# Optimization experiments

Measured on AMD Instinct MI355X. Metric: run time of the kernel, lower is better.

## Reference

```python
import jax, jax.numpy as jnp
import numpy as np

B, L, D, H = 2, 8192, 1024, 16
HD = D // H  # head_dim = 64


def setup_inputs() -> dict:
    key = jax.random.key(0)
    ks = jax.random.split(key, 5)
    s = 1.0 / np.sqrt(D)
    return {
        "x": jax.random.normal(ks[0], (B, L, D), dtype=jnp.float32),
        "Wq": jax.random.normal(ks[1], (D, D), dtype=jnp.float32) * s,
        "bq": jnp.zeros((D,), dtype=jnp.float32),
        "Wk": jax.random.normal(ks[2], (D, D), dtype=jnp.float32) * s,
        "bk": jnp.zeros((D,), dtype=jnp.float32),
        "Wv": jax.random.normal(ks[3], (D, D), dtype=jnp.float32) * s,
        "bv": jnp.zeros((D,), dtype=jnp.float32),
        "Wo": jax.random.normal(ks[4], (D, D), dtype=jnp.float32) * s,
        "bo": jnp.zeros((D,), dtype=jnp.float32),
    }


def _rotary(seq_len, dim):
    pos = jnp.arange(seq_len, dtype=jnp.float32)
    freq = 1.0 / (10000.0 ** (jnp.arange(0, dim, 2, dtype=jnp.float32) / dim))
    ang = pos[:, None] * freq[None, :]               # (L, dim/2)
    sin, cos = jnp.sin(ang), jnp.cos(ang)
    # interleave-duplicate: stack((s,s),-1).reshape(L,dim)  (matches torch code)
    sin = jnp.stack((sin, sin), axis=-1).reshape(seq_len, dim)
    cos = jnp.stack((cos, cos), axis=-1).reshape(seq_len, dim)
    return sin, cos


def _rotate_half(t):
    t1, t2 = jnp.split(t, 2, axis=-1)
    return jnp.concatenate([-t2, t1], axis=-1)


def reference(x, Wq, bq, Wk, bk, Wv, bv, Wo, bo):
    b, l, d = x.shape
    q = (x @ Wq + bq).reshape(b, l, H, HD)
    k = (x @ Wk + bk).reshape(b, l, H, HD)
    v = (x @ Wv + bv).reshape(b, l, H, HD)

    sin, cos = _rotary(l, HD)
    sin = sin[None, :, None, :]  # (1, L, 1, HD)
    cos = cos[None, :, None, :]
    q = q * cos + _rotate_half(q) * sin
    k = k * cos + _rotate_half(k) * sin

    # NOTE: faithful to original — heads NOT transposed to (B,H,L,HD),
    # so scores are (B, L, H, H): attention mixes across heads per position.
    scores = jnp.einsum('blhd,bled->blhe', q, k) / jnp.sqrt(jnp.float32(HD))
    w = jax.nn.softmax(scores, axis=-1)              # dropout = identity (eval)
    out = jnp.einsum('blhe,bled->blhd', w, v).reshape(b, l, d)
    return out @ Wo + bo
```

## Files before the change

kernel.cpp:

```cpp
#include <hip/hip_runtime.h>
#include <hip/hip_bf16.h>

typedef __bf16 bf16_t;
typedef __bf16 bf16x8 __attribute__((ext_vector_type(8)));
typedef float f32x4 __attribute__((ext_vector_type(4)));

#define SEQ_L 8192
#define DMODEL 1024
#define NHEAD 16
#define HDIM 64
static constexpr int MROWS = 2 * SEQ_L;

__device__ __forceinline__ void async_cp16(const bf16_t* g, bf16_t* l) {
  __builtin_amdgcn_global_load_lds(
      (__attribute__((address_space(1))) void*)(void*)(g),
      (__attribute__((address_space(3))) void*)(void*)(l), 16, 0, 0);
}
__device__ __forceinline__ void wg_barrier() { __builtin_amdgcn_s_barrier(); }

__global__ __launch_bounds__(256) void f32_to_bf16_k(const float* __restrict__ in,
                                                     bf16_t* __restrict__ out, int n) {
  int i = (blockIdx.x * 256 + threadIdx.x) * 8;
  if (i >= n) return;
  float4 a = *(const float4*)(in + i);
  float4 b = *(const float4*)(in + i + 4);
  bf16x8 o;
  o[0] = (__bf16)a.x; o[1] = (__bf16)a.y; o[2] = (__bf16)a.z; o[3] = (__bf16)a.w;
  o[4] = (__bf16)b.x; o[5] = (__bf16)b.y; o[6] = (__bf16)b.z; o[7] = (__bf16)b.w;
  *(bf16x8*)(out + i) = o;
}

__global__ __launch_bounds__(256) void w_to_bt_k(
    const float* __restrict__ W0, const float* __restrict__ W1,
    const float* __restrict__ W2, const float* __restrict__ W3,
    bf16_t* __restrict__ T0, bf16_t* __restrict__ T1,
    bf16_t* __restrict__ T2, bf16_t* __restrict__ T3) {
  __shared__ float tile[32][33];
  const int z = blockIdx.z;
  const float* W = (z == 0) ? W0 : (z == 1) ? W1 : (z == 2) ? W2 : W3;
  bf16_t* T = (z == 0) ? T0 : (z == 1) ? T1 : (z == 2) ? T2 : T3;
  const int bx = blockIdx.x, by = blockIdx.y;
  const int tx = threadIdx.x, ty = threadIdx.y;
#pragma unroll
  for (int r = 0; r < 4; ++r)
    tile[ty + r * 8][tx] = W[(size_t)(by * 32 + ty + r * 8) * DMODEL + bx * 32 + tx];
  __syncthreads();
#pragma unroll
  for (int r = 0; r < 4; ++r)
    T[(size_t)(bx * 32 + ty + r * 8) * DMODEL + by * 32 + tx] = (bf16_t)tile[tx][ty + r * 8];
}

__global__ __launch_bounds__(256) void rope_tab_k(float2* __restrict__ tab) {
  int i = blockIdx.x * 256 + threadIdx.x;
  int pos = i >> 5, j = i & 31;
  double freq = pow(10000.0, -(double)j / 32.0);
  double ang = (double)pos * freq;
  tab[i] = make_float2((float)cos(ang), (float)sin(ang));
}

template <int MODE>
__global__ __launch_bounds__(512, 2) void gemm256(
    const bf16_t* __restrict__ A, const bf16_t* __restrict__ Bt,
    const float* __restrict__ b0, const float* __restrict__ b1,
    const float* __restrict__ b2, const float2* __restrict__ rope,
    void* __restrict__ O0, void* __restrict__ O1, void* __restrict__ O2) {
  constexpr int K = DMODEL;
  constexpr int KT = K / 64;
  __shared__ bf16_t As_[2][256 * 64];
  __shared__ bf16_t Bs_[2][256 * 64];
  const int tid = threadIdx.x;
  const int lane = tid & 63;
  const int wave = tid >> 6;
  const int wm = wave >> 2;
  const int wn = wave & 3;
  const size_t row0 = (size_t)blockIdx.x * 256;
  const int col0 = blockIdx.y * 256;
  const int fr = lane & 15;
  const int fkb = (lane >> 4) * 16;

  const int srow = tid >> 3;
  const int schunk = (tid & 7) ^ ((tid >> 3) & 7);
  const bf16_t* gA = A + (row0 + srow) * K + schunk * 8;
  const bf16_t* gB = Bt + ((size_t)col0 + srow) * K + schunk * 8;

#define STAGE_A(j, h)                                  \
  do {                                                 \
    const bf16_t* _g = gA + ((h)*128) * K + (j)*64;    \
    bf16_t* _l = &As_[(j)&1][(h)*8192 + tid * 8];      \
    async_cp16(_g, _l);                                \
    async_cp16(_g + 64 * K, _l + 4096);                \
  } while (0)
#define STAGE_B(j, h)                                  \
  do {                                                 \
    const bf16_t* _g = gB + ((h)*128) * K + (j)*64;    \
    bf16_t* _l = &Bs_[(j)&1][(h)*8192 + tid * 8];      \
    async_cp16(_g, _l);                                \
    async_cp16(_g + 64 * K, _l + 4096);                \
  } while (0)
#define RD(base, row, kh)                                                    \
  (*(const bf16x8*)((const char*)(base) +                                    \
                    (((row)*128 + ((kh)*64 + fkb)) ^ (((row)&7) << 4))))
#define VMCNT(n) asm volatile("s_waitcnt vmcnt(" #n ")")

  f32x4 acc[8][4] = {};
  bf16x8 af[4][2], bf0[2][2], bf1[2][2];

  STAGE_A(0, 0); STAGE_A(0, 1);
  STAGE_B(0, 0); STAGE_B(0, 1);
  STAGE_B(1, 0); STAGE_B(1, 1);
  STAGE_A(1, 0);
  VMCNT(6);
  wg_barrier();

  for (int m = 0; m < KT; ++m) {
    const bf16_t* Ac = &As_[m & 1][0];
    const bf16_t* Bc = &Bs_[m & 1][0];
#pragma unroll
    for (int f = 0; f < 4; ++f) {
      const int r = wm * 128 + f * 16 + fr;
      af[f][0] = RD(Ac, r, 0);
      af[f][1] = RD(Ac, r, 1);
    }
#pragma unroll
    for (int f = 0; f < 2; ++f) {
      const int r = wn * 64 + f * 16 + fr;
      bf0[f][0] = RD(Bc, r, 0);
      bf0[f][1] = RD(Bc, r, 1);
    }
    if (m + 1 < KT) STAGE_A(m + 1, 1);
    wg_barrier();
    __builtin_amdgcn_s_setprio(1);
#pragma unroll
    for (int f = 0; f < 4; ++f)
#pragma unroll
      for (int n = 0; n < 2; ++n)
#pragma unroll
        for (int kh = 0; kh < 2; ++kh)
          acc[f][n] = __builtin_amdgcn_mfma_f32_16x16x32_bf16(af[f][kh], bf0[n][kh], acc[f][n], 0, 0, 0);
    __builtin_amdgcn_s_setprio(0);
    wg_barrier();
#pragma unroll
    for (int f = 0; f < 2; ++f) {
      const int r = wn * 64 + (2 + f) * 16 + fr;
      bf1[f][0] = RD(Bc, r, 0);
      bf1[f][1] = RD(Bc, r, 1);
    }
    wg_barrier();
    __builtin_amdgcn_s_setprio(1);
#pragma unroll
    for (int f = 0; f < 4; ++f)
#pragma unroll
      for (int n = 0; n < 2; ++n)
#pragma unroll
        for (int kh = 0; kh < 2; ++kh)
          acc[f][2 + n] = __builtin_amdgcn_mfma_f32_16x16x32_bf16(af[f][kh], bf1[n][kh], acc[f][2 + n], 0, 0, 0);
    __builtin_amdgcn_s_setprio(0);
    wg_barrier();
#pragma unroll
    for (int f = 0; f < 4; ++f) {
      const int r = wm * 128 + (4 + f) * 16 + fr;
      af[f][0] = RD(Ac, r, 0);
      af[f][1] = RD(Ac, r, 1);
    }
    if (m + 2 < KT) STAGE_B(m + 2, 0);
    wg_barrier();
    __builtin_amdgcn_s_setprio(1);
#pragma unroll
    for (int f = 0; f < 4; ++f)
#pragma unroll
      for (int n = 0; n < 2; ++n)
#pragma unroll
        for (int kh = 0; kh < 2; ++kh)
          acc[4 + f][2 + n] = __builtin_amdgcn_mfma_f32_16x16x32_bf16(af[f][kh], bf1[n][kh], acc[4 + f][2 + n], 0, 0, 0);
    __builtin_amdgcn_s_setprio(0);
    wg_barrier();
    if (m + 2 < KT) {
      STAGE_B(m + 2, 1);
      STAGE_A(m + 2, 0);
      VMCNT(6);
    } else if (m + 1 < KT) {
      VMCNT(0);
    }
    wg_barrier();
    __builtin_amdgcn_s_setprio(1);
#pragma unroll
    for (int f = 0; f < 4; ++f)
#pragma unroll
      for (int n = 0; n < 2; ++n)
#pragma unroll
        for (int kh = 0; kh < 2; ++kh)
          acc[4 + f][n] = __builtin_amdgcn_mfma_f32_16x16x32_bf16(af[f][kh], bf0[n][kh], acc[4 + f][n], 0, 0, 0);
    __builtin_amdgcn_s_setprio(0);
    wg_barrier();
  }
#undef STAGE_A
#undef STAGE_B
#undef RD
#undef VMCNT

  const int lr = (lane >> 4) * 4;
  const int lc = lane & 15;
  const int gcol = col0 + wn * 64;
  int which = 0;
  const float* bias = b0;
  int ocol = gcol;
  if constexpr (MODE == 0) {
    which = gcol >> 10;
    bias = (which == 0) ? b0 : (which == 1) ? b1 : b2;
    ocol = gcol - (which << 10);
  }
  const bool do_rope = (MODE == 0) && (which < 2);
  bf16_t* Cb = nullptr;
  float* Cf = nullptr;
  if constexpr (MODE == 0)
    Cb = (bf16_t*)((which == 0) ? O0 : (which == 1) ? O1 : O2);
  else
    Cf = (float*)O0;

#pragma unroll
  for (int mf = 0; mf < 8; ++mf) {
#pragma unroll
    for (int i = 0; i < 4; ++i) {
      const size_t grow = row0 + wm * 128 + mf * 16 + lr + i;
      float vv[4];
#pragma unroll
      for (int n = 0; n < 4; ++n) vv[n] = acc[mf][n][i] + bias[ocol + n * 16 + lc];
      if (do_rope) {
        const int pos = (int)(grow & (size_t)(SEQ_L - 1));
        const float2* rp = rope + (size_t)pos * 32 + (lc >> 1);
        float rv[4];
#pragma unroll
        for (int n = 0; n < 4; ++n) {
          float2 cs = rp[n * 8];
          rv[n] = (n < 2) ? vv[n] * cs.x - vv[n + 2] * cs.y
                          : vv[n] * cs.x + vv[n - 2] * cs.y;
        }
#pragma unroll
        for (int n = 0; n < 4; ++n) vv[n] = rv[n];
      }
      const size_t cbase = grow * (size_t)DMODEL + ocol + lc;
      if constexpr (MODE == 1) {
#pragma unroll
        for (int n = 0; n < 4; ++n) Cf[cbase + n * 16] = vv[n];
      } else {
#pragma unroll
        for (int n = 0; n < 4; ++n) Cb[cbase + n * 16] = (bf16_t)vv[n];
      }
    }
  }
}

__global__ __launch_bounds__(256) void attn_heads_k(const bf16_t* __restrict__ qb,
                                                    const bf16_t* __restrict__ kb,
                                                    const bf16_t* __restrict__ vb,
                                                    bf16_t* __restrict__ ob) {
  const int t = blockIdx.x * 256 + threadIdx.x;
  const int row = t >> 4;
  const int h = t & 15;
  const size_t rbase = (size_t)row * DMODEL;

  float q[HDIM];
#pragma unroll
  for (int j = 0; j < 8; ++j) {
    bf16x8 v8 = *(const bf16x8*)(qb + rbase + h * HDIM + j * 8);
#pragma unroll
    for (int u = 0; u < 8; ++u) q[j * 8 + u] = (float)v8[u];
  }
  float s[NHEAD];
#pragma unroll
  for (int e = 0; e < NHEAD; ++e) {
    float a = 0.f;
#pragma unroll
    for (int j = 0; j < 8; ++j) {
      bf16x8 k8 = *(const bf16x8*)(kb + rbase + e * HDIM + j * 8);
#pragma unroll
      for (int u = 0; u < 8; ++u) a += q[j * 8 + u] * (float)k8[u];
    }
    s[e] = a * 0.125f;
  }
  float mx = s[0];
#pragma unroll
  for (int e = 1; e < NHEAD; ++e) mx = fmaxf(mx, s[e]);
  float sum = 0.f;
#pragma unroll
  for (int e = 0; e < NHEAD; ++e) {
    s[e] = __expf(s[e] - mx);
    sum += s[e];
  }
  const float inv = 1.f / sum;
  float o[HDIM] = {};
#pragma unroll
  for (int e = 0; e < NHEAD; ++e) {
    const float w = s[e] * inv;
#pragma unroll
    for (int j = 0; j < 8; ++j) {
      bf16x8 v8 = *(const bf16x8*)(vb + rbase + e * HDIM + j * 8);
#pragma unroll
      for (int u = 0; u < 8; ++u) o[j * 8 + u] += w * (float)v8[u];
    }
  }
#pragma unroll
  for (int j = 0; j < 8; ++j) {
    bf16x8 st;
#pragma unroll
    for (int u = 0; u < 8; ++u) st[u] = (__bf16)o[j * 8 + u];
    *(bf16x8*)(ob + rbase + h * HDIM + j * 8) = st;
  }
}

extern "C" void kernel_launch(void* const* d_in, const int* in_sizes, int n_in,
                              void* d_out, int out_size, void* d_ws, size_t ws_size,
                              hipStream_t stream) {
  const float* x = (const float*)d_in[0];
  const float* Wq = (const float*)d_in[1];
  const float* bq = (const float*)d_in[2];
  const float* Wk = (const float*)d_in[3];
  const float* bk = (const float*)d_in[4];
  const float* Wv = (const float*)d_in[5];
  const float* bv = (const float*)d_in[6];
  const float* Wo = (const float*)d_in[7];
  const float* bo = (const float*)d_in[8];

  const int M = MROWS, N = DMODEL, K = DMODEL;

  char* p = (char*)d_ws;
  bf16_t* xb = (bf16_t*)p;    p += (size_t)M * K * 2;
  bf16_t* Wqkvt = (bf16_t*)p; p += (size_t)3 * N * K * 2;
  bf16_t* Wot = (bf16_t*)p;   p += (size_t)N * K * 2;
  bf16_t* qb = (bf16_t*)p;    p += (size_t)M * N * 2;
  bf16_t* kb = (bf16_t*)p;    p += (size_t)M * N * 2;
  bf16_t* vb = (bf16_t*)p;    p += (size_t)M * N * 2;
  bf16_t* ab = (bf16_t*)p;    p += (size_t)M * N * 2;
  float2* rope = (float2*)p;  p += (size_t)SEQ_L * 32 * sizeof(float2);

  bf16_t* Wqt = Wqkvt;
  bf16_t* Wkt = Wqkvt + (size_t)N * K;
  bf16_t* Wvt = Wqkvt + (size_t)2 * N * K;

  f32_to_bf16_k<<<(M * K) / (256 * 8), 256, 0, stream>>>(x, xb, M * K);
  w_to_bt_k<<<dim3(32, 32, 4), dim3(32, 8), 0, stream>>>(Wq, Wk, Wv, Wo, Wqt, Wkt, Wvt, Wot);
  rope_tab_k<<<(SEQ_L * 32) / 256, 256, 0, stream>>>(rope);

  gemm256<0><<<dim3(M / 256, (3 * N) / 256), 512, 0, stream>>>(
      xb, Wqkvt, bq, bk, bv, rope, (void*)qb, (void*)kb, (void*)vb);
  attn_heads_k<<<(M * NHEAD) / 256, 256, 0, stream>>>(qb, kb, vb, ab);
  gemm256<1><<<dim3(M / 256, N / 256), 512, 0, stream>>>(
      ab, Wot, bo, nullptr, nullptr, nullptr, d_out, nullptr, nullptr);
}
```

Before: 246.4 us.

## Simplify GEMM main loop to load full tile then run all MFMAs

Replaces the four-phase interleaved GEMM K-loop, where LDS reads, MFMA blocks and async global-to-LDS staging alternated between many barriers, with a simpler schedule. Each iteration now reads all A and B fragments from LDS, issues all 64 MFMAs, then stages the full next-next tile and waits. Scheduling fences are added to stop the compiler from reordering across the phases. This removes several workgroup barriers per iteration but holds more fragment registers live and gives up fine-grained overlap of global loads with compute.

```diff
diff --git a/kernel.cpp b/kernel.cpp
--- a/kernel.cpp
+++ b/kernel.cpp
@@ -97,106 +97,80 @@
     async_cp16(_g, _l);                                \
     async_cp16(_g + 64 * K, _l + 4096);                \
   } while (0)
+#define STAGE_T(j)                                     \
+  do {                                                 \
+    STAGE_A(j, 0); STAGE_A(j, 1);                      \
+    STAGE_B(j, 0); STAGE_B(j, 1);                      \
+  } while (0)
 #define RD(base, row, kh)                                                    \
   (*(const bf16x8*)((const char*)(base) +                                    \
                     (((row)*128 + ((kh)*64 + fkb)) ^ (((row)&7) << 4))))
 #define VMCNT(n) asm volatile("s_waitcnt vmcnt(" #n ")")
+#define SCHED_FENCE() __builtin_amdgcn_sched_barrier(0)
 
   f32x4 acc[8][4] = {};
-  bf16x8 af[4][2], bf0[2][2], bf1[2][2];
-
-  STAGE_A(0, 0); STAGE_A(0, 1);
-  STAGE_B(0, 0); STAGE_B(0, 1);
-  STAGE_B(1, 0); STAGE_B(1, 1);
-  STAGE_A(1, 0);
-  VMCNT(6);
+  bf16x8 a0[4][2], a1[4][2], bfr[4][2];
+
+  STAGE_T(0);
+  STAGE_T(1);
+  VMCNT(8);
   wg_barrier();
+  SCHED_FENCE();
 
   for (int m = 0; m < KT; ++m) {
     const bf16_t* Ac = &As_[m & 1][0];
     const bf16_t* Bc = &Bs_[m & 1][0];
 #pragma unroll
     for (int f = 0; f < 4; ++f) {
+      const int r = wn * 64 + f * 16 + fr;
+      bfr[f][0] = RD(Bc, r, 0);
+      bfr[f][1] = RD(Bc, r, 1);
+    }
+#pragma unroll
+    for (int f = 0; f < 4; ++f) {
       const int r = wm * 128 + f * 16 + fr;
-      af[f][0] = RD(Ac, r, 0);
-      af[f][1] = RD(Ac, r, 1);
-    }
-#pragma unroll
-    for (int f = 0; f < 2; ++f) {
-      const int r = wn * 64 + f * 16 + fr;
-      bf0[f][0] = RD(Bc, r, 0);
-      bf0[f][1] = RD(Bc, r, 1);
-    }
-    if (m + 1 < KT) STAGE_A(m + 1, 1);
-    wg_barrier();
+      a0[f][0] = RD(Ac, r, 0);
+      a0[f][1] = RD(Ac, r, 1);
+    }
+#pragma unroll
+    for (int f = 0; f < 4; ++f) {
+      const int r = wm * 128 + (4 + f) * 16 + fr;
+      a1[f][0] = RD(Ac, r, 0);
+      a1[f][1] = RD(Ac, r, 1);
+    }
     __builtin_amdgcn_s_setprio(1);
 #pragma unroll
     for (int f = 0; f < 4; ++f)
 #pragma unroll
-      for (int n = 0; n < 2; ++n)
+      for (int n = 0; n < 4; ++n)
 #pragma unroll
         for (int kh = 0; kh < 2; ++kh)
-          acc[f][n] = __builtin_amdgcn_mfma_f32_16x16x32_bf16(af[f][kh], bf0[n][kh], acc[f][n], 0, 0, 0);
+          acc[f][n] = __builtin_amdgcn_mfma_f32_16x16x32_bf16(a0[f][kh], bfr[n][kh], acc[f][n], 0, 0, 0);
+#pragma unroll
+    for (int f = 0; f < 4; ++f)
+#pragma unroll
+      for (int n = 0; n < 4; ++n)
+#pragma unroll
+        for (int kh = 0; kh < 2; ++kh)
+          acc[4 + f][n] = __builtin_amdgcn_mfma_f32_16x16x32_bf16(a1[f][kh], bfr[n][kh], acc[4 + f][n], 0, 0, 0);
     __builtin_amdgcn_s_setprio(0);
     wg_barrier();
-#pragma unroll
-    for (int f = 0; f < 2; ++f) {
-      const int r = wn * 64 + (2 + f) * 16 + fr;
-      bf1[f][0] = RD(Bc, r, 0);
-      bf1[f][1] = RD(Bc, r, 1);
+    SCHED_FENCE();
+    if (m + 2 < KT) {
+      STAGE_T(m + 2);
+      VMCNT(8);
+    } else {
+      VMCNT(0);
     }
     wg_barrier();
-    __builtin_amdgcn_s_setprio(1);
-#pragma unroll
-    for (int f = 0; f < 4; ++f)
-#pragma unroll
-      for (int n = 0; n < 2; ++n)
-#pragma unroll
-        for (int kh = 0; kh < 2; ++kh)
-          acc[f][2 + n] = __builtin_amdgcn_mfma_f32_16x16x32_bf16(af[f][kh], bf1[n][kh], acc[f][2 + n], 0, 0, 0);
-    __builtin_amdgcn_s_setprio(0);
-    wg_barrier();
-#pragma unroll
-    for (int f = 0; f < 4; ++f) {
-      const int r = wm * 128 + (4 + f) * 16 + fr;
-      af[f][0] = RD(Ac, r, 0);
-      af[f][1] = RD(Ac, r, 1);
-    }
-    if (m + 2 < KT) STAGE_B(m + 2, 0);
-    wg_barrier();
-    __builtin_amdgcn_s_setprio(1);
-#pragma unroll
-    for (int f = 0; f < 4; ++f)
-#pragma unroll
-      for (int n = 0; n < 2; ++n)
-#pragma unroll
-        for (int kh = 0; kh < 2; ++kh)
-          acc[4 + f][2 + n] = __builtin_amdgcn_mfma_f32_16x16x32_bf16(af[f][kh], bf1[n][kh], acc[4 + f][2 + n], 0, 0, 0);
-    __builtin_amdgcn_s_setprio(0);
-    wg_barrier();
-    if (m + 2 < KT) {
-      STAGE_B(m + 2, 1);
-      STAGE_A(m + 2, 0);
-      VMCNT(6);
-    } else if (m + 1 < KT) {
-      VMCNT(0);
-    }
-    wg_barrier();
-    __builtin_amdgcn_s_setprio(1);
-#pragma unroll
-    for (int f = 0; f < 4; ++f)
-#pragma unroll
-      for (int n = 0; n < 2; ++n)
-#pragma unroll
-        for (int kh = 0; kh < 2; ++kh)
-          acc[4 + f][n] = __builtin_amdgcn_mfma_f32_16x16x32_bf16(af[f][kh], bf0[n][kh], acc[4 + f][n], 0, 0, 0);
-    __builtin_amdgcn_s_setprio(0);
-    wg_barrier();
+    SCHED_FENCE();
   }
 #undef STAGE_A
 #undef STAGE_B
+#undef STAGE_T
 #undef RD
 #undef VMCNT
+#undef SCHED_FENCE
 
   const int lr = (lane >> 4) * 4;
   const int lc = lane & 15;
```

Result: no change. 245.6 us (-0.3%).
